# Kernel tuning notes

Hardware: AMD Instinct MI355X
Metric: run time of the kernel (lower is better)

Reference implementation:

```python
import jax, jax.numpy as jnp
import numpy as np

N_NODES = 100000
N_EDGES = 3200000


def _gat_conv(x, src, dst, ea, Wx, We, a_src, a_dst, a_edge, b, n):
    # PyG GATConv, heads=1, edge_dim set: h = x@Wx^T, he = ea@We^T
    h = x @ Wx.T                      # [N,16]
    he = ea @ We.T                    # [E,16]
    alpha = h[src] @ a_src + h[dst] @ a_dst + he @ a_edge  # [E]
    alpha = jnp.where(alpha > 0, alpha, 0.2 * alpha)       # leaky_relu(0.2)
    m = jax.ops.segment_max(alpha, dst, num_segments=n)
    m = jnp.where(jnp.isfinite(m), m, 0.0)
    ex = jnp.exp(alpha - m[dst])
    s = jax.ops.segment_sum(ex, dst, num_segments=n)
    a = ex / (s[dst] + 1e-16)
    out = jax.ops.segment_sum(a[:, None] * h[src], dst, num_segments=n)
    return out + b


def setup_inputs() -> dict:
    key = jax.random.key(0)
    ks = iter(jax.random.split(key, 40))
    rn = lambda shape, s=0.1: jax.random.normal(next(ks), shape, dtype=jnp.float32) * s
    inp = {}
    inp['x'] = jax.random.normal(next(ks), (N_NODES, 4), dtype=jnp.float32)
    inp['edge_index'] = jax.random.randint(next(ks), (2, N_EDGES), 0, N_NODES, dtype=jnp.int64)
    inp['edge_attr'] = jax.random.normal(next(ks), (N_EDGES, 6), dtype=jnp.float32)
    # conv1: GATConv(4->16, edge_dim=6)
    inp['c1_Wx'] = rn((16, 4)); inp['c1_We'] = rn((16, 6))
    inp['c1_asrc'] = rn((16,)); inp['c1_adst'] = rn((16,)); inp['c1_aedge'] = rn((16,))
    inp['c1_b'] = rn((16,))
    # edge1 MLP: 38->32->64->32->16
    inp['e1_w1'] = rn((32, 38)); inp['e1_b1'] = rn((32,))
    inp['e1_w2'] = rn((64, 32)); inp['e1_b2'] = rn((64,))
    inp['e1_w3'] = rn((32, 64)); inp['e1_b3'] = rn((32,))
    inp['e1_w4'] = rn((16, 32)); inp['e1_b4'] = rn((16,))
    # conv2: GATConv(16->16, edge_dim=16)
    inp['c2_Wx'] = rn((16, 16)); inp['c2_We'] = rn((16, 16))
    inp['c2_asrc'] = rn((16,)); inp['c2_adst'] = rn((16,)); inp['c2_aedge'] = rn((16,))
    inp['c2_b'] = rn((16,))
    # node head 16->16->2, edge head 16->16->4
    inp['nl_w1'] = rn((16, 16)); inp['nl_b1'] = rn((16,))
    inp['nl_w2'] = rn((2, 16)); inp['nl_b2'] = rn((2,))
    inp['el_w1'] = rn((16, 16)); inp['el_b1'] = rn((16,))
    inp['el_w2'] = rn((4, 16)); inp['el_b2'] = rn((4,))
    return inp


def reference(x, edge_index, edge_attr,
              c1_Wx, c1_We, c1_asrc, c1_adst, c1_aedge, c1_b,
              e1_w1, e1_b1, e1_w2, e1_b2, e1_w3, e1_b3, e1_w4, e1_b4,
              c2_Wx, c2_We, c2_asrc, c2_adst, c2_aedge, c2_b,
              nl_w1, nl_b1, nl_w2, nl_b2,
              el_w1, el_b1, el_w2, el_b2):
    n = x.shape[0]
    src, dst = edge_index[0], edge_index[1]
    x1 = _gat_conv(x, src, dst, edge_attr, c1_Wx, c1_We, c1_asrc, c1_adst, c1_aedge, c1_b, n)
    # edge MLP on [x_src | edge_attr | x_dst] (dropout = identity in eval)
    e = jnp.concatenate([x1[src], edge_attr, x1[dst]], axis=1)  # [E,38]
    e = jax.nn.relu(e @ e1_w1.T + e1_b1)
    e = jax.nn.relu(e @ e1_w2.T + e1_b2)
    e = jax.nn.relu(e @ e1_w3.T + e1_b3)
    e = e @ e1_w4.T + e1_b4                                     # [E,16]
    x2 = _gat_conv(x1, src, dst, e, c2_Wx, c2_We, c2_asrc, c2_adst, c2_aedge, c2_b, n)
    node = jax.nn.relu(jax.nn.relu(x2 @ nl_w1.T + nl_b1) @ nl_w2.T + nl_b2)
    edge = jax.nn.relu(jax.nn.relu(e @ el_w1.T + el_b1) @ el_w2.T + el_b2)
    return (jax.nn.log_softmax(node, axis=1), jax.nn.log_softmax(edge, axis=1))
```

## Files before the change

kernel.cpp:

```cpp
#include <hip/hip_runtime.h>

#define NN 100000
#define NE 3200000
#define NB 98

typedef unsigned int u32;
typedef unsigned short u16;
typedef _Float16 f16x2 __attribute__((ext_vector_type(2)));
typedef __fp16 fp16v2 __attribute__((ext_vector_type(2)));

__device__ __forceinline__ int clampi(int s){
  s = s < 0 ? 0 : s;
  return s >= NN ? NN-1 : s;
}

__device__ __forceinline__ f16x2 pk2(float x, float y){
  fp16v2 r = __builtin_amdgcn_cvt_pkrtz(x, y);
  return __builtin_bit_cast(f16x2, r);
}
__device__ __forceinline__ float dot2(f16x2 a, f16x2 b, float c){
  return __builtin_amdgcn_fdot2(a, b, c, false);
}
__device__ __forceinline__ float f16lo(u32 w){
  __fp16 h = __builtin_bit_cast(__fp16, (u16)(w & 0xffffu));
  return (float)h;
}
__device__ __forceinline__ float f16hi(u32 w){
  __fp16 h = __builtin_bit_cast(__fp16, (u16)(w >> 16));
  return (float)h;
}
__device__ __forceinline__ float f16u(u16 w){
  __fp16 h = __builtin_bit_cast(__fp16, w);
  return (float)h;
}

template<int N4>
__device__ __forceinline__ float dotl(const float* __restrict__ a, const float* w){
  float acc0 = 0.f, acc1 = 0.f;
  #pragma unroll
  for (int k = 0; k < N4; k += 2){
    float4 q0 = ((const float4*)w)[k];
    acc0 += a[4*k]*q0.x + a[4*k+1]*q0.y + a[4*k+2]*q0.z + a[4*k+3]*q0.w;
    float4 q1 = ((const float4*)w)[k+1];
    acc1 += a[4*k+4]*q1.x + a[4*k+5]*q1.y + a[4*k+6]*q1.z + a[4*k+7]*q1.w;
  }
  return acc0 + acc1;
}

__global__ __launch_bounds__(256,8) void khist(const int* __restrict__ ei, int* __restrict__ cnt){
  int i = blockIdx.x*256 + threadIdx.x;
  if (i >= NE) return;
  atomicAdd(&cnt[clampi(ei[NE+i])], 1);
}

__global__ __launch_bounds__(1024) void kscanA(const int* __restrict__ cnt, int* __restrict__ bsum){
  __shared__ int wsum[16];
  int tid = threadIdx.x;
  int i = blockIdx.x*1024 + tid;
  int x = (i < NN) ? cnt[i] : 0;
  #pragma unroll
  for (int ofs = 1; ofs < 64; ofs <<= 1) x += __shfl_xor(x, ofs, 64);
  if ((tid & 63) == 0) wsum[tid >> 6] = x;
  __syncthreads();
  if (tid == 0){
    int t = 0;
    #pragma unroll
    for (int k = 0; k < 16; k++) t += wsum[k];
    bsum[blockIdx.x] = t;
  }
}

__global__ void kscanB(const int* __restrict__ bsum, int* __restrict__ boff, int* __restrict__ offN){
  if (threadIdx.x == 0){
    int c = 0;
    for (int b = 0; b < NB; b++){ boff[b] = c; c += bsum[b]; }
    offN[0] = c;
  }
}

__global__ __launch_bounds__(1024) void kscanC(int* __restrict__ cnt, const int* __restrict__ boff,
                                               int* __restrict__ off){
  __shared__ int wsum[16];
  int tid = threadIdx.x;
  int i = blockIdx.x*1024 + tid;
  int v = (i < NN) ? cnt[i] : 0;
  int x = v;
  #pragma unroll
  for (int ofs = 1; ofs < 64; ofs <<= 1){
    int t = __shfl_up(x, ofs, 64);
    if ((tid & 63) >= ofs) x += t;
  }
  if ((tid & 63) == 63) wsum[tid >> 6] = x;
  __syncthreads();
  if (tid < 16){
    int y = wsum[tid];
    #pragma unroll
    for (int ofs = 1; ofs < 16; ofs <<= 1){
      int t = __shfl_up(y, ofs, 64);
      if (tid >= ofs) y += t;
    }
    wsum[tid] = y;
  }
  __syncthreads();
  int wb = (tid >= 64) ? wsum[(tid >> 6) - 1] : 0;
  if (i < NN){ off[i] = boff[blockIdx.x] + wb + x - v; cnt[i] = 0; }
}

__global__ __launch_bounds__(256,4) void k1(const float* __restrict__ x,
    const float* __restrict__ Wx, const float* __restrict__ asrc, const float* __restrict__ adst,
    float* __restrict__ hs1, float* __restrict__ hd1)
{
  __shared__ float wL[64], aS[16], aD[16];
  int tid = threadIdx.x;
  if (tid < 64) wL[tid] = Wx[tid];
  if (tid < 16){ aS[tid] = asrc[tid]; aD[tid] = adst[tid]; }
  __syncthreads();
  int n = blockIdx.x*256 + tid;
  if (n >= NN) return;
  float4 xr = ((const float4*)x)[n];
  float hs=0.f, hd=0.f;
  #pragma unroll
  for (int j=0;j<16;j++){
    float h = xr.x*wL[j*4+0] + xr.y*wL[j*4+1] + xr.z*wL[j*4+2] + xr.w*wL[j*4+3];
    hs += h*aS[j]; hd += h*aD[j];
  }
  hs1[n]=hs; hd1[n]=hd;
}

__global__ __launch_bounds__(256,8) void k2a(const int* __restrict__ ei,
    const float* __restrict__ ea, const float* __restrict__ We, const float* __restrict__ aedge,
    const float* __restrict__ hs1, const float* __restrict__ hd1,
    const int* __restrict__ off, int* __restrict__ cnt, float2* __restrict__ edata)
{
  __shared__ float w6[6];
  int tid = threadIdx.x;
  if (tid < 6){
    float acc = 0.f;
    for (int j=0;j<16;j++) acc += aedge[j] * We[j*6+tid];
    w6[tid] = acc;
  }
  __syncthreads();
  int i = blockIdx.x*256 + tid;
  if (i >= NE) return;
  int s = clampi(ei[i]);
  int d = clampi(ei[NE + i]);
  const float2* eap = (const float2*)ea + (size_t)i*3;
  float2 u0 = eap[0], u1 = eap[1], u2 = eap[2];
  float al = hs1[s] + hd1[d]
    + u0.x*w6[0] + u0.y*w6[1] + u1.x*w6[2]
    + u1.y*w6[3] + u2.x*w6[4] + u2.y*w6[5];
  al = al > 0.f ? al : 0.2f*al;
  float ex = __expf(al);
  int pos = off[d] + atomicAdd(&cnt[d], 1);
  edata[pos] = make_float2(ex, __int_as_float(s));
}

__global__ __launch_bounds__(256,8) void kaggx(const float2* __restrict__ edata,
    const int* __restrict__ off, const float* __restrict__ x,
    float* __restrict__ acc4, float* __restrict__ s, int* __restrict__ cnt)
{
  int t = blockIdx.x*256 + threadIdx.x;
  int n = t >> 4;
  int j = t & 15;
  if (n >= NN) return;
  int f = j & 3, ks = j >> 2;
  int beg = off[n], end = off[n+1];
  float aj = 0.f, sl = 0.f;
  for (int k = beg + ks; k < end; k += 4){
    float2 p = edata[k];
    int src = __float_as_int(p.y);
    aj += p.x * x[(size_t)src*4 + f];
    sl += p.x;
  }
  aj += __shfl_xor(aj, 4, 64); aj += __shfl_xor(aj, 8, 64);
  sl += __shfl_xor(sl, 4, 64); sl += __shfl_xor(sl, 8, 64);
  if (ks == 0) acc4[(size_t)n*4 + f] = aj;
  if (j == 0){ s[n] = sl; cnt[n] = 0; }
}

__global__ __launch_bounds__(256,2) void k4(const float* __restrict__ acc4,
    const float* __restrict__ sb, const float* __restrict__ c1b,
    const float* __restrict__ Wx1, const float* __restrict__ Wx2,
    const float* __restrict__ a2s, const float* __restrict__ a2d,
    const float* __restrict__ w1p,
    u32* __restrict__ hpk,
    float* __restrict__ hs2, float* __restrict__ hd2,
    u32* __restrict__ uh, u32* __restrict__ vh)
{
  __shared__ float wL[256], bL[16], aS[16], aD[16], w0L[64];
  __shared__ float w1sL[32*16], w1dL[32*16];
  int tid = threadIdx.x;
  wL[tid] = Wx2[tid];
  if (tid < 64) w0L[tid] = Wx1[tid];
  if (tid < 16){ bL[tid]=c1b[tid]; aS[tid]=a2s[tid]; aD[tid]=a2d[tid]; }
  for (int idx=tid; idx<512; idx+=256){
    int j=idx>>4, k=idx&15;
    w1sL[idx] = w1p[j*38+k];
    w1dL[idx] = w1p[j*38+22+k];
  }
  __syncthreads();
  int n = blockIdx.x*256 + tid;
  if (n >= NN) return;
  float inv = 1.f/(sb[n] + 1e-16f);
  float4 a4 = ((const float4*)acc4)[n];
  float m0 = a4.x*inv, m1 = a4.y*inv, m2 = a4.z*inv, m3 = a4.w*inv;
  float xv[16];
  #pragma unroll
  for (int j=0;j<16;j++)
    xv[j] = m0*w0L[j*4+0] + m1*w0L[j*4+1] + m2*w0L[j*4+2] + m3*w0L[j*4+3] + bL[j];
  float hs=0.f, hd=0.f;
  float hv[16];
  #pragma unroll
  for (int j=0;j<16;j++){
    float acc = 0.f;
    #pragma unroll
    for (int k=0;k<16;k++) acc += xv[k]*wL[j*16+k];
    hv[j] = acc; hs += acc*aS[j]; hd += acc*aD[j];
  }
  u32* hr = hpk + (size_t)n*8;
  #pragma unroll
  for (int j=0;j<8;j++) hr[j] = __builtin_bit_cast(u32, pk2(hv[2*j], hv[2*j+1]));
  hs2[n]=hs; hd2[n]=hd;
  u32* ur = uh + (size_t)n*16;
  u32* vr = vh + (size_t)n*16;
  #pragma unroll
  for (int j=0;j<16;j++){
    float u0 = dotl<4>(xv, &w1sL[(2*j)*16]);
    float u1 = dotl<4>(xv, &w1sL[(2*j+1)*16]);
    ur[j] = __builtin_bit_cast(u32, pk2(u0, u1));
    float v0 = dotl<4>(xv, &w1dL[(2*j)*16]);
    float v1 = dotl<4>(xv, &w1dL[(2*j+1)*16]);
    vr[j] = __builtin_bit_cast(u32, pk2(v0, v1));
  }
}

__global__ __launch_bounds__(256,5) void k5(
    const int* __restrict__ ei, const float* __restrict__ ea,
    const u32* __restrict__ uh, const u32* __restrict__ vh,
    const float* __restrict__ hs2, const float* __restrict__ hd2,
    const float* w1p, const float* b1p, const float* w2p, const float* b2p,
    const float* w3p, const float* b3p, const float* w4p, const float* b4p,
    const float* We2, const float* a2e,
    const float* ew1p, const float* eb1p, const float* ew2p, const float* eb2p,
    const int* __restrict__ off, int* __restrict__ cnt, float2* __restrict__ edata,
    float* __restrict__ eout)
{
  __shared__ __align__(16) f16x2 w1eh[32*4];  __shared__ float b1L[32];
  __shared__ __align__(16) f16x2 w2h[64*16];  __shared__ float b2L[64];
  __shared__ __align__(16) f16x2 w3h[32*32];  __shared__ float b3L[32];
  __shared__ __align__(16) f16x2 w4h[16*16];  __shared__ float b4L[16];
  __shared__ __align__(16) f16x2 ew1h[16*8];  __shared__ float eb1L[16];
  __shared__ __align__(16) f16x2 ew2h[4*8];   __shared__ float eb2L[4];
  __shared__ __align__(16) f16x2 w16h[8];
  int tid = threadIdx.x;
  if (tid < 128){
    int j=tid>>2, kk=tid&3;
    int k0=2*kk, k1=2*kk+1;
    float v0 = (k0<6) ? w1p[j*38+16+k0] : 0.f;
    float v1 = (k1<6) ? w1p[j*38+16+k1] : 0.f;
    w1eh[tid] = pk2(v0, v1);
  }
  for (int idx=tid; idx<1024; idx+=256){
    int j=idx>>4, kk=idx&15;
    w2h[idx] = pk2(w2p[j*32+2*kk], w2p[j*32+2*kk+1]);
  }
  for (int idx=tid; idx<1024; idx+=256){
    int j=idx>>5, kk=idx&31;
    w3h[idx] = pk2(w3p[j*64+2*kk], w3p[j*64+2*kk+1]);
  }
  if (tid < 256){
    int j=tid>>4, kk=tid&15;
    w4h[tid] = pk2(w4p[j*32+2*kk], w4p[j*32+2*kk+1]);
  }
  if (tid < 128){
    int j=tid>>3, kk=tid&7;
    ew1h[tid] = pk2(ew1p[j*16+2*kk], ew1p[j*16+2*kk+1]);
  }
  if (tid < 32){
    int j=tid>>3, kk=tid&7;
    ew2h[tid] = pk2(ew2p[j*16+2*kk], ew2p[j*16+2*kk+1]);
  }
  if (tid < 8){
    float s0=0.f, s1=0.f;
    for (int j=0;j<16;j++){
      s0 += a2e[j] * We2[j*16 + 2*tid];
      s1 += a2e[j] * We2[j*16 + 2*tid + 1];
    }
    w16h[tid] = pk2(s0, s1);
  }
  if (tid < 64) b2L[tid] = b2p[tid];
  if (tid < 32){ b1L[tid] = b1p[tid]; b3L[tid] = b3p[tid]; }
  if (tid < 16){ b4L[tid] = b4p[tid]; eb1L[tid] = eb1p[tid]; }
  if (tid < 4)  eb2L[tid] = eb2p[tid];
  __syncthreads();

  int i = blockIdx.x*256 + tid;
  if (i >= NE) return;
  int s = clampi(ei[i]);
  int d = clampi(ei[NE + i]);

  f16x2 a1h[16];
  {
    const float2* eap = (const float2*)ea + (size_t)i*3;
    float2 e0=eap[0], e1=eap[1], e2=eap[2];
    f16x2 eh[4];
    eh[0]=pk2(e0.x,e0.y); eh[1]=pk2(e1.x,e1.y); eh[2]=pk2(e2.x,e2.y); eh[3]=pk2(0.f,0.f);
    const uint4* up = (const uint4*)(uh + (size_t)s*16);
    const uint4* vp = (const uint4*)(vh + (size_t)d*16);
    uint4 U[4], V[4];
    #pragma unroll
    for (int q=0;q<4;q++){ U[q]=up[q]; V[q]=vp[q]; }
    u32 uw[16], vw[16];
    #pragma unroll
    for (int q=0;q<4;q++){
      uw[4*q]=U[q].x; uw[4*q+1]=U[q].y; uw[4*q+2]=U[q].z; uw[4*q+3]=U[q].w;
      vw[4*q]=V[q].x; vw[4*q+1]=V[q].y; vw[4*q+2]=V[q].z; vw[4*q+3]=V[q].w;
    }
    #pragma unroll
    for (int j=0;j<16;j++){
      float t0 = b1L[2*j]   + f16lo(uw[j]) + f16lo(vw[j]);
      float t1 = b1L[2*j+1] + f16hi(uw[j]) + f16hi(vw[j]);
      #pragma unroll
      for (int kk=0;kk<4;kk++){
        t0 = dot2(eh[kk], w1eh[(2*j)*4+kk],   t0);
        t1 = dot2(eh[kk], w1eh[(2*j+1)*4+kk], t1);
      }
      a1h[j] = pk2(fmaxf(t0,0.f), fmaxf(t1,0.f));
    }
  }
  f16x2 a2h[32];
  #pragma unroll
  for (int j=0;j<32;j++){
    float acc0 = b2L[2*j], acc1 = b2L[2*j+1];
    #pragma unroll
    for (int kk=0;kk<16;kk++){
      acc0 = dot2(a1h[kk], w2h[(2*j)*16+kk],   acc0);
      acc1 = dot2(a1h[kk], w2h[(2*j+1)*16+kk], acc1);
    }
    a2h[j] = pk2(fmaxf(acc0,0.f), fmaxf(acc1,0.f));
  }
  f16x2 a3h[16];
  #pragma unroll
  for (int j=0;j<16;j++){
    float acc0 = b3L[2*j], acc1 = b3L[2*j+1];
    #pragma unroll
    for (int kk=0;kk<32;kk++){
      acc0 = dot2(a2h[kk], w3h[(2*j)*32+kk],   acc0);
      acc1 = dot2(a2h[kk], w3h[(2*j+1)*32+kk], acc1);
    }
    a3h[j] = pk2(fmaxf(acc0,0.f), fmaxf(acc1,0.f));
  }
  f16x2 eh4[8];
  #pragma unroll
  for (int j=0;j<8;j++){
    float acc0 = b4L[2*j], acc1 = b4L[2*j+1];
    #pragma unroll
    for (int kk=0;kk<16;kk++){
      acc0 = dot2(a3h[kk], w4h[(2*j)*16+kk],   acc0);
      acc1 = dot2(a3h[kk], w4h[(2*j+1)*16+kk], acc1);
    }
    eh4[j] = pk2(acc0, acc1);
  }
  f16x2 th[8];
  #pragma unroll
  for (int j=0;j<8;j++){
    float acc0 = eb1L[2*j], acc1 = eb1L[2*j+1];
    #pragma unroll
    for (int kk=0;kk<8;kk++){
      acc0 = dot2(eh4[kk], ew1h[(2*j)*8+kk],   acc0);
      acc1 = dot2(eh4[kk], ew1h[(2*j+1)*8+kk], acc1);
    }
    th[j] = pk2(fmaxf(acc0,0.f), fmaxf(acc1,0.f));
  }
  float y0 = eb2L[0], y1 = eb2L[1], y2 = eb2L[2], y3 = eb2L[3];
  #pragma unroll
  for (int kk=0;kk<8;kk++){
    y0 = dot2(th[kk], ew2h[0*8+kk], y0);
    y1 = dot2(th[kk], ew2h[1*8+kk], y1);
    y2 = dot2(th[kk], ew2h[2*8+kk], y2);
    y3 = dot2(th[kk], ew2h[3*8+kk], y3);
  }
  y0 = fmaxf(y0,0.f); y1 = fmaxf(y1,0.f); y2 = fmaxf(y2,0.f); y3 = fmaxf(y3,0.f);
  float m = fmaxf(fmaxf(y0,y1), fmaxf(y2,y3));
  float l = m + __logf(__expf(y0-m)+__expf(y1-m)+__expf(y2-m)+__expf(y3-m));
  float4 eo; eo.x = y0-l; eo.y = y1-l; eo.z = y2-l; eo.w = y3-l;
  ((float4*)eout)[i] = eo;

  float al = hs2[s] + hd2[d];
  #pragma unroll
  for (int kk=0;kk<8;kk++) al = dot2(eh4[kk], w16h[kk], al);
  al = al > 0.f ? al : 0.2f*al;
  float ex = __expf(al);
  int pos = off[d] + atomicAdd(&cnt[d], 1);
  edata[pos] = make_float2(ex, __int_as_float(s));
}

__global__ __launch_bounds__(256,8) void kagg2(const float2* __restrict__ edata,
    const int* __restrict__ off, const u16* __restrict__ hpk,
    const float* __restrict__ c2b,
    const float* __restrict__ w1p, const float* __restrict__ b1p,
    const float* __restrict__ w2p, const float* __restrict__ b2p,
    float* __restrict__ nout, int* __restrict__ cnt)
{
  __shared__ float w1L[256], cb[16], b1L[16], w2L[32], b2L[2];
  int tid = threadIdx.x;
  w1L[tid] = w1p[tid];
  if (tid < 16){ cb[tid] = c2b[tid]; b1L[tid] = b1p[tid]; }
  if (tid < 32) w2L[tid] = w2p[tid];
  if (tid < 2)  b2L[tid] = b2p[tid];
  __syncthreads();
  int t = blockIdx.x*256 + tid;
  int n = t >> 6;
  int l = t & 63;
  if (n >= NN) return;
  int j = l & 15, ks = l >> 4;
  int beg = off[n], end = off[n+1];
  float aj = 0.f, sl = 0.f;
  for (int k = beg + ks; k < end; k += 4){
    float2 p = edata[k];
    int src = __float_as_int(p.y);
    aj += p.x * f16u(hpk[(size_t)src*16 + j]);
    sl += p.x;
  }
  aj += __shfl_xor(aj, 16, 64); aj += __shfl_xor(aj, 32, 64);
  sl += __shfl_xor(sl, 16, 64); sl += __shfl_xor(sl, 32, 64);
  float inv = 1.f/(sl + 1e-16f);
  float vj = aj*inv + cb[j];
  float tj = b1L[j];
  #pragma unroll
  for (int k=0;k<16;k++){
    float vk = __shfl(vj, k, 16);
    tj += vk * w1L[j*16 + k];
  }
  tj = fmaxf(tj, 0.f);
  float p0 = tj * w2L[j];
  float p1 = tj * w2L[16 + j];
  #pragma unroll
  for (int ofs=1; ofs<16; ofs<<=1){
    p0 += __shfl_xor(p0, ofs, 64);
    p1 += __shfl_xor(p1, ofs, 64);
  }
  if (l == 0){
    float y0 = fmaxf(p0 + b2L[0], 0.f);
    float y1 = fmaxf(p1 + b2L[1], 0.f);
    float m = fmaxf(y0, y1);
    float lg = m + __logf(__expf(y0-m) + __expf(y1-m));
    float2 no; no.x = y0-lg; no.y = y1-lg;
    ((float2*)nout)[n] = no;
    cnt[n] = 0;
  }
}

extern "C" void kernel_launch(void* const* d_in, const int* in_sizes, int n_in,
                              void* d_out, int out_size, void* d_ws, size_t ws_size,
                              hipStream_t stream)
{
  const float* x  = (const float*)d_in[0];
  const int* ei   = (const int*)d_in[1];
  const float* ea = (const float*)d_in[2];
  const float* c1Wx = (const float*)d_in[3];
  const float* c1We = (const float*)d_in[4];
  const float* c1as = (const float*)d_in[5];
  const float* c1ad = (const float*)d_in[6];
  const float* c1ae = (const float*)d_in[7];
  const float* c1b  = (const float*)d_in[8];
  const float* e1w1 = (const float*)d_in[9];
  const float* e1b1 = (const float*)d_in[10];
  const float* e1w2 = (const float*)d_in[11];
  const float* e1b2 = (const float*)d_in[12];
  const float* e1w3 = (const float*)d_in[13];
  const float* e1b3 = (const float*)d_in[14];
  const float* e1w4 = (const float*)d_in[15];
  const float* e1b4 = (const float*)d_in[16];
  const float* c2Wx = (const float*)d_in[17];
  const float* c2We = (const float*)d_in[18];
  const float* c2as = (const float*)d_in[19];
  const float* c2ad = (const float*)d_in[20];
  const float* c2ae = (const float*)d_in[21];
  const float* c2b  = (const float*)d_in[22];
  const float* nlw1 = (const float*)d_in[23];
  const float* nlb1 = (const float*)d_in[24];
  const float* nlw2 = (const float*)d_in[25];
  const float* nlb2 = (const float*)d_in[26];
  const float* elw1 = (const float*)d_in[27];
  const float* elb1 = (const float*)d_in[28];
  const float* elw2 = (const float*)d_in[29];
  const float* elb2 = (const float*)d_in[30];

  float* ws = (float*)d_ws;
  const size_t N = NN;
  int* off   = (int*)ws;
  int* cnt   = (int*)ws + (N + 8);
  int* bsum  = (int*)ws + (2*N + 8);
  int* boff  = (int*)ws + (2*N + 136);
  u32* hpk   = (u32*)(ws + 2*N + 264);
  float* hs  = ws + 10*N + 264;
  float* hd  = hs + N;
  float* acc4= hd + N;
  float* s   = acc4 + 4*N;
  u32* uh    = (u32*)(s + N);
  u32* vh    = uh + 16*N;
  float2* edata = (float2*)(vh + 16*N);

  float* nout = (float*)d_out;
  float* eout = (float*)d_out + 200000;

  const int GE = (NE + 255)/256;
  const int GN = (NN + 255)/256;

  (void)hipMemsetAsync(cnt, 0, N*sizeof(int), stream);
  khist<<<GE, 256, 0, stream>>>(ei, cnt);
  kscanA<<<NB, 1024, 0, stream>>>(cnt, bsum);
  kscanB<<<1, 64, 0, stream>>>(bsum, boff, off + NN);
  kscanC<<<NB, 1024, 0, stream>>>(cnt, boff, off);
  k1<<<GN, 256, 0, stream>>>(x, c1Wx, c1as, c1ad, hs, hd);
  k2a<<<GE, 256, 0, stream>>>(ei, ea, c1We, c1ae, hs, hd, off, cnt, edata);
  kaggx<<<(NN*16 + 255)/256, 256, 0, stream>>>(edata, off, x, acc4, s, cnt);
  k4<<<GN, 256, 0, stream>>>(acc4, s, c1b, c1Wx, c2Wx, c2as, c2ad, e1w1, hpk, hs, hd, uh, vh);
  k5<<<GE, 256, 0, stream>>>(ei, ea, uh, vh, hs, hd,
      e1w1, e1b1, e1w2, e1b2, e1w3, e1b3, e1w4, e1b4,
      c2We, c2ae, elw1, elb1, elw2, elb2,
      off, cnt, edata, eout);
  kagg2<<<(NN*64 + 255)/256, 256, 0, stream>>>(edata, off, (const u16*)hpk,
      c2b, nlw1, nlb1, nlw2, nlb2, nout, cnt);
}
```

Baseline: 760.3 us.

## Fuse conv1 aggregation with node transform into one 16-lane-per-node kernel

```diff
diff --git a/kernel.cpp b/kernel.cpp
--- a/kernel.cpp
+++ b/kernel.cpp
@@ -32,19 +32,6 @@
 __device__ __forceinline__ float f16u(u16 w){
   __fp16 h = __builtin_bit_cast(__fp16, w);
   return (float)h;
-}
-
-template<int N4>
-__device__ __forceinline__ float dotl(const float* __restrict__ a, const float* w){
-  float acc0 = 0.f, acc1 = 0.f;
-  #pragma unroll
-  for (int k = 0; k < N4; k += 2){
-    float4 q0 = ((const float4*)w)[k];
-    acc0 += a[4*k]*q0.x + a[4*k+1]*q0.y + a[4*k+2]*q0.z + a[4*k+3]*q0.w;
-    float4 q1 = ((const float4*)w)[k+1];
-    acc1 += a[4*k+4]*q1.x + a[4*k+5]*q1.y + a[4*k+6]*q1.z + a[4*k+7]*q1.w;
-  }
-  return acc0 + acc1;
 }
 
 __global__ __launch_bounds__(256,8) void khist(const int* __restrict__ ei, int* __restrict__ cnt){
@@ -155,11 +142,27 @@
   edata[pos] = make_float2(ex, __int_as_float(s));
 }
 
-__global__ __launch_bounds__(256,8) void kaggx(const float2* __restrict__ edata,
+__global__ __launch_bounds__(256,8) void k34(const float2* __restrict__ edata,
     const int* __restrict__ off, const float* __restrict__ x,
-    float* __restrict__ acc4, float* __restrict__ s, int* __restrict__ cnt)
-{
-  int t = blockIdx.x*256 + threadIdx.x;
+    const float* __restrict__ c1b, const float* __restrict__ Wx1, const float* __restrict__ Wx2,
+    const float* __restrict__ a2s, const float* __restrict__ a2d,
+    const float* __restrict__ w1p,
+    u32* __restrict__ hpk, float* __restrict__ hs2, float* __restrict__ hd2,
+    u32* __restrict__ uh, u32* __restrict__ vh, int* __restrict__ cnt)
+{
+  __shared__ float w0L[64], bL[16], wL[256], aS[16], aD[16];
+  __shared__ float w1sL[32*16], w1dL[32*16];
+  int tid = threadIdx.x;
+  wL[tid] = Wx2[tid];
+  if (tid < 64) w0L[tid] = Wx1[tid];
+  if (tid < 16){ bL[tid]=c1b[tid]; aS[tid]=a2s[tid]; aD[tid]=a2d[tid]; }
+  for (int idx=tid; idx<512; idx+=256){
+    int j=idx>>4, k=idx&15;
+    w1sL[idx] = w1p[j*38+k];
+    w1dL[idx] = w1p[j*38+22+k];
+  }
+  __syncthreads();
+  int t = blockIdx.x*256 + tid;
   int n = t >> 4;
   int j = t & 15;
   if (n >= NN) return;
@@ -174,67 +177,35 @@
   }
   aj += __shfl_xor(aj, 4, 64); aj += __shfl_xor(aj, 8, 64);
   sl += __shfl_xor(sl, 4, 64); sl += __shfl_xor(sl, 8, 64);
-  if (ks == 0) acc4[(size_t)n*4 + f] = aj;
-  if (j == 0){ s[n] = sl; cnt[n] = 0; }
-}
-
-__global__ __launch_bounds__(256,2) void k4(const float* __restrict__ acc4,
-    const float* __restrict__ sb, const float* __restrict__ c1b,
-    const float* __restrict__ Wx1, const float* __restrict__ Wx2,
-    const float* __restrict__ a2s, const float* __restrict__ a2d,
-    const float* __restrict__ w1p,
-    u32* __restrict__ hpk,
-    float* __restrict__ hs2, float* __restrict__ hd2,
-    u32* __restrict__ uh, u32* __restrict__ vh)
-{
-  __shared__ float wL[256], bL[16], aS[16], aD[16], w0L[64];
-  __shared__ float w1sL[32*16], w1dL[32*16];
-  int tid = threadIdx.x;
-  wL[tid] = Wx2[tid];
-  if (tid < 64) w0L[tid] = Wx1[tid];
-  if (tid < 16){ bL[tid]=c1b[tid]; aS[tid]=a2s[tid]; aD[tid]=a2d[tid]; }
-  for (int idx=tid; idx<512; idx+=256){
-    int j=idx>>4, k=idx&15;
-    w1sL[idx] = w1p[j*38+k];
-    w1dL[idx] = w1p[j*38+22+k];
-  }
-  __syncthreads();
-  int n = blockIdx.x*256 + tid;
-  if (n >= NN) return;
-  float inv = 1.f/(sb[n] + 1e-16f);
-  float4 a4 = ((const float4*)acc4)[n];
-  float m0 = a4.x*inv, m1 = a4.y*inv, m2 = a4.z*inv, m3 = a4.w*inv;
-  float xv[16];
-  #pragma unroll
-  for (int j=0;j<16;j++)
-    xv[j] = m0*w0L[j*4+0] + m1*w0L[j*4+1] + m2*w0L[j*4+2] + m3*w0L[j*4+3] + bL[j];
-  float hs=0.f, hd=0.f;
-  float hv[16];
-  #pragma unroll
-  for (int j=0;j<16;j++){
-    float acc = 0.f;
-    #pragma unroll
-    for (int k=0;k<16;k++) acc += xv[k]*wL[j*16+k];
-    hv[j] = acc; hs += acc*aS[j]; hd += acc*aD[j];
-  }
-  u32* hr = hpk + (size_t)n*8;
-  #pragma unroll
-  for (int j=0;j<8;j++) hr[j] = __builtin_bit_cast(u32, pk2(hv[2*j], hv[2*j+1]));
-  hs2[n]=hs; hd2[n]=hd;
-  u32* ur = uh + (size_t)n*16;
-  u32* vr = vh + (size_t)n*16;
-  #pragma unroll
-  for (int j=0;j<16;j++){
-    float u0 = dotl<4>(xv, &w1sL[(2*j)*16]);
-    float u1 = dotl<4>(xv, &w1sL[(2*j+1)*16]);
-    ur[j] = __builtin_bit_cast(u32, pk2(u0, u1));
-    float v0 = dotl<4>(xv, &w1dL[(2*j)*16]);
-    float v1 = dotl<4>(xv, &w1dL[(2*j+1)*16]);
-    vr[j] = __builtin_bit_cast(u32, pk2(v0, v1));
-  }
-}
-
-__global__ __launch_bounds__(256,5) void k5(
+  float inv = 1.f/(sl + 1e-16f);
+  float m0 = __shfl(aj, 0, 16)*inv;
+  float m1 = __shfl(aj, 1, 16)*inv;
+  float m2 = __shfl(aj, 2, 16)*inv;
+  float m3 = __shfl(aj, 3, 16)*inv;
+  float xvj = m0*w0L[j*4+0] + m1*w0L[j*4+1] + m2*w0L[j*4+2] + m3*w0L[j*4+3] + bL[j];
+  float hv = 0.f, u0=0.f, u1=0.f, v0=0.f, v1=0.f;
+  #pragma unroll
+  for (int k=0;k<16;k++){
+    float vk = __shfl(xvj, k, 16);
+    hv += vk * wL[j*16+k];
+    u0 += vk * w1sL[(2*j)*16+k];
+    u1 += vk * w1sL[(2*j+1)*16+k];
+    v0 += vk * w1dL[(2*j)*16+k];
+    v1 += vk * w1dL[(2*j+1)*16+k];
+  }
+  ((u16*)hpk)[(size_t)n*16 + j] = (u16)(__builtin_bit_cast(u32, pk2(hv, 0.f)) & 0xffffu);
+  uh[(size_t)n*16 + j] = __builtin_bit_cast(u32, pk2(u0, u1));
+  vh[(size_t)n*16 + j] = __builtin_bit_cast(u32, pk2(v0, v1));
+  float hsp = hv*aS[j], hdp = hv*aD[j];
+  #pragma unroll
+  for (int ofs=1; ofs<16; ofs<<=1){
+    hsp += __shfl_xor(hsp, ofs, 64);
+    hdp += __shfl_xor(hdp, ofs, 64);
+  }
+  if (j == 0){ hs2[n]=hsp; hd2[n]=hdp; cnt[n]=0; }
+}
+
+__global__ __launch_bounds__(256,8) void k5(
     const int* __restrict__ ei, const float* __restrict__ ea,
     const u32* __restrict__ uh, const u32* __restrict__ vh,
     const float* __restrict__ hs2, const float* __restrict__ hd2,
@@ -496,9 +467,7 @@
   u32* hpk   = (u32*)(ws + 2*N + 264);
   float* hs  = ws + 10*N + 264;
   float* hd  = hs + N;
-  float* acc4= hd + N;
-  float* s   = acc4 + 4*N;
-  u32* uh    = (u32*)(s + N);
+  u32* uh    = (u32*)(hd + N);
   u32* vh    = uh + 16*N;
   float2* edata = (float2*)(vh + 16*N);
 
@@ -515,8 +484,8 @@
   kscanC<<<NB, 1024, 0, stream>>>(cnt, boff, off);
   k1<<<GN, 256, 0, stream>>>(x, c1Wx, c1as, c1ad, hs, hd);
   k2a<<<GE, 256, 0, stream>>>(ei, ea, c1We, c1ae, hs, hd, off, cnt, edata);
-  kaggx<<<(NN*16 + 255)/256, 256, 0, stream>>>(edata, off, x, acc4, s, cnt);
-  k4<<<GN, 256, 0, stream>>>(acc4, s, c1b, c1Wx, c2Wx, c2as, c2ad, e1w1, hpk, hs, hd, uh, vh);
+  k34<<<(NN*16 + 255)/256, 256, 0, stream>>>(edata, off, x,
+      c1b, c1Wx, c2Wx, c2as, c2ad, e1w1, hpk, hs, hd, uh, vh, cnt);
   k5<<<GE, 256, 0, stream>>>(ei, ea, uh, vh, hs, hd,
       e1w1, e1b1, e1w2, e1b2, e1w3, e1b3, e1w4, e1b4,
       c2We, c2ae, elw1, elb1, elw2, elb2,
```

Measured after the change: 766.7 us. Within noise of the previous version (+0.8%).
